# Kernel optimization log

Measured on AMD Instinct MI355X. Metric: run time of the kernel, lower is better.

## Reference

```python
import jax, jax.numpy as jnp
import numpy as np

H, DH, PE = 8, 64, 32
SCALE = DH ** -0.5


def setup_inputs() -> dict:
    key = jax.random.key(0)
    ks = jax.random.split(key, 12)
    B, L, D, K, G = 2, 4096, 256, 16, 4
    inner = H * DH
    kv_in = D + PE
    return {
        "spatial": jax.random.normal(ks[0], (B, L, D), jnp.float32),
        "topk_indices": jax.random.randint(ks[1], (B, L, K), 0, L, jnp.int32),
        "rpe": jax.random.normal(ks[2], (B, L, K, PE), jnp.float32),
        "self_rpe": jax.random.normal(ks[3], (B, L, 1, PE), jnp.float32),
        "distances": jax.random.uniform(ks[4], (B, L, K), jnp.float32) * 10.0,
        "global_latents": jax.random.normal(ks[5], (B, G, D), jnp.float32),
        "Wq": jax.random.normal(ks[6], (D, inner), jnp.float32) * (D ** -0.5),
        "Wk": jax.random.normal(ks[7], (kv_in, inner), jnp.float32) * (kv_in ** -0.5),
        "Wv": jax.random.normal(ks[8], (kv_in, inner), jnp.float32) * (kv_in ** -0.5),
        "Wo": jax.random.normal(ks[9], (inner, D), jnp.float32) * (inner ** -0.5),
        "bo": jnp.zeros((D,), jnp.float32),
        "log_sigma": jnp.full((H,), np.log(3.0), jnp.float32),
        "global_bias": jnp.zeros((), jnp.float32),
    }


def reference(spatial, topk_indices, rpe, self_rpe, distances, global_latents,
              Wq, Wk, Wv, Wo, bo, log_sigma, global_bias):
    B, L, D = spatial.shape
    k = topk_indices.shape[-1]
    G = global_latents.shape[1]
    dt = spatial.dtype

    # gather per-query neighbor features: [B, L, k, D]
    neighbors = jax.vmap(lambda s, idx: s[idx])(spatial, topk_indices)

    # context = [self, neighbors, globals] -> [B, L, c, D], c = 1 + k + G
    ctx = jnp.concatenate([
        spatial[:, :, None, :],
        neighbors,
        jnp.broadcast_to(global_latents[:, None, :, :], (B, L, G, D)),
    ], axis=2)

    # RPE concat on feature dim (self_rpe, rpe, zeros for globals)
    rpe_cat = jnp.concatenate([
        self_rpe, rpe, jnp.zeros((B, L, G, PE), dt)
    ], axis=2)
    ctx = jnp.concatenate([ctx, rpe_cat], axis=-1)  # [B, L, c, D+PE]

    Q = (spatial @ Wq).reshape(B, L, H, DH).transpose(0, 2, 1, 3)          # bhld
    Kt = (ctx @ Wk).reshape(B, L, 1 + k + G, H, DH).transpose(0, 3, 1, 2, 4)  # bhlcd
    Vt = (ctx @ Wv).reshape(B, L, 1 + k + G, H, DH).transpose(0, 3, 1, 2, 4)

    attn = jnp.einsum('bhld,bhlcd->bhlc', Q, Kt) * SCALE

    # gaussian distance bias on local (self + k neighbors) slots
    sigma_sq = jnp.exp(log_sigma) ** 2                     # [H]
    dist_local = jnp.concatenate([jnp.zeros((B, L, 1), dt), distances], axis=2)  # [B,L,1+k]
    gauss = -(dist_local ** 2)[:, None, :, :] / (2.0 * sigma_sq[None, :, None, None])
    bias = jnp.concatenate([
        gauss,
        jnp.broadcast_to(global_bias, (B, H, L, G)).astype(dt),
    ], axis=-1)
    attn = attn + bias

    w = jax.nn.softmax(attn, axis=-1)
    out = jnp.einsum('bhlc,bhlcd->bhld', w, Vt)
    out = out.transpose(0, 2, 1, 3).reshape(B, L, H * DH)
    return out @ Wo + bo
```

## Files before the change

### kernel.cpp

```cpp
#include <hip/hip_runtime.h>
#include <hip/hip_bf16.h>

#define BB 2
#define LL 4096
#define DD 256
#define KK 16
#define GG 4
#define HH 8
#define DH 64
#define PE 32
#define INNER 512
#define CC 21
#define MM (BB*LL)
#define SCALE 0.125f
#define NT1 1792
#define KT1 256
#define NT2 256
#define KT2 768

typedef unsigned short u16;
typedef __attribute__((ext_vector_type(8))) short bf16x8;
typedef __attribute__((ext_vector_type(4))) float f32x4;
typedef unsigned short ushort4_t __attribute__((ext_vector_type(4)));
typedef unsigned short ushort8_t __attribute__((ext_vector_type(8)));

static __device__ __forceinline__ float bf2f(unsigned short u) {
    return __uint_as_float(((unsigned)u) << 16);
}
static __device__ __forceinline__ unsigned short f2bf(float f) {
    unsigned u = __float_as_uint(f);
    unsigned r = u + 0x7fffu + ((u >> 16) & 1u);
    return (unsigned short)(r >> 16);
}
static __device__ __forceinline__ void gld_lds16(const void* g, void* l) {
    __builtin_amdgcn_global_load_lds(
        (const __attribute__((address_space(1))) unsigned int*)g,
        (__attribute__((address_space(3))) unsigned int*)l, 16, 0, 0);
}

static __device__ __forceinline__ float red8_dpp(float x) {
    int xi = __float_as_int(x);
    x += __int_as_float(__builtin_amdgcn_update_dpp(0, xi, 0xB1, 0xF, 0xF, true));
    xi = __float_as_int(x);
    x += __int_as_float(__builtin_amdgcn_update_dpp(0, xi, 0x4E, 0xF, 0xF, true));
    xi = __float_as_int(x);
    x += __int_as_float(__builtin_amdgcn_update_dpp(0, xi, 0x141, 0xF, 0xF, true));
    return x;
}

__global__ __launch_bounds__(256) void megaprep1(
    const float* __restrict__ Wq, const float* __restrict__ Wk,
    const float* __restrict__ Wv, const float* __restrict__ Wo,
    const float* __restrict__ spatial, const float* __restrict__ gl,
    float* __restrict__ A, float* __restrict__ M2, u16* __restrict__ Sb,
    u16* __restrict__ Kg, u16* __restrict__ Vg)
{
    const int bid = blockIdx.x;
    const int tid = threadIdx.x;
    __shared__ float smem[INNER];

    if (bid < 256) {
        const int e = bid;
        smem[tid]       = Wq[e * INNER + tid];
        smem[tid + 256] = Wq[e * INNER + 256 + tid];
        __syncthreads();
        const int h = tid >> 5, p = tid & 31;
        const float* __restrict__ wr = &Wk[(size_t)(DD + p) * INNER + h * DH];
        const float* __restrict__ qh = &smem[h * DH];
        float s = 0.f;
        #pragma unroll 8
        for (int d = 0; d < DH; ++d) s += wr[d] * qh[d];
        A[e * 256 + tid] = s;
    } else if (bid < 512) {
        const int hp = bid - 256;
        const int h = hp >> 5, p = hp & 31;
        if (tid < DH) smem[tid] = Wv[(size_t)(DD + p) * INNER + h * DH + tid];
        __syncthreads();
        float s = 0.f;
        #pragma unroll 8
        for (int d = 0; d < DH; ++d) s += smem[d] * Wo[(size_t)(h * DH + d) * DD + tid];
        M2[hp * 256 + tid] = s;
    } else if (bid < 1536) {
        const size_t i = ((size_t)(bid - 512) * 256 + tid) * 8;
        float4 a = *reinterpret_cast<const float4*>(&spatial[i]);
        float4 b = *reinterpret_cast<const float4*>(&spatial[i + 4]);
        ushort8_t v = { f2bf(a.x), f2bf(a.y), f2bf(a.z), f2bf(a.w),
                        f2bf(b.x), f2bf(b.y), f2bf(b.z), f2bf(b.w) };
        *reinterpret_cast<ushort8_t*>(&Sb[i]) = v;
    } else {
        const int local = bid - 1536;
        const int bg = local >> 2;
        const int col = (local & 3) * 128 + (tid & 127);
        const bool isv = tid >= 128;
        const float* __restrict__ W = isv ? Wv : Wk;
        const float* __restrict__ x = &gl[bg * DD];
        float s = 0.f;
        #pragma unroll 4
        for (int k = 0; k < DD; ++k) s += x[k] * W[(size_t)k * INNER + col];
        if (isv) Vg[bg * INNER + col] = f2bf(s);
        else     Kg[bg * INNER + col] = f2bf(s);
    }
}

__global__ __launch_bounds__(256) void megaprep2(
    const float* __restrict__ Wq, const float* __restrict__ Wk,
    const float* __restrict__ Wv, const float* __restrict__ A,
    const float* __restrict__ Wo, const float* __restrict__ M2,
    u16* __restrict__ Wt, u16* __restrict__ Wot)
{
    __shared__ float tile[64][65];
    const int bid = blockIdx.x;
    const int tid = threadIdx.x;

    const float* src; int ld, nloc, n0, k0, ldo; u16* dstbase; int kt;
    if (bid < 112) {
        n0 = (bid % 28) * 64; k0 = (bid / 28) * 64;
        if (n0 < 512)       { src = Wq; ld = INNER; nloc = n0; }
        else if (n0 < 1024) { src = Wk; ld = INNER; nloc = n0 - 512; }
        else if (n0 < 1536) { src = Wv; ld = INNER; nloc = n0 - 1024; }
        else                { src = A;  ld = 256;   nloc = n0 - 1536; }
        dstbase = Wt; ldo = KT1; kt = k0;
    } else {
        const int local = bid - 112;
        n0 = (local % 4) * 64; k0 = (local / 4) * 64;
        if (k0 < 512) { src = Wo; kt = k0; }
        else          { src = M2; kt = k0 - 512; }
        ld = DD; nloc = n0;
        dstbase = Wot; ldo = KT2;
    }

    const int tk = tid >> 4;
    const int tn = (tid & 15) * 4;
    #pragma unroll
    for (int rep = 0; rep < 4; ++rep) {
        const int k = kt + tk + rep * 16;
        float4 v = *reinterpret_cast<const float4*>(&src[(size_t)k * ld + nloc + tn]);
        tile[tk + rep * 16][tn + 0] = v.x; tile[tk + rep * 16][tn + 1] = v.y;
        tile[tk + rep * 16][tn + 2] = v.z; tile[tk + rep * 16][tn + 3] = v.w;
    }
    __syncthreads();
    const int wn = tid >> 2;
    const int wk = (tid & 3) * 16;
    ushort8_t o0, o1;
    #pragma unroll
    for (int i = 0; i < 8; ++i) o0[i] = f2bf(tile[wk + i][wn]);
    #pragma unroll
    for (int i = 0; i < 8; ++i) o1[i] = f2bf(tile[wk + 8 + i][wn]);
    u16* dst = &dstbase[(size_t)(n0 + wn) * ldo + k0 + wk];
    *reinterpret_cast<ushort8_t*>(dst)     = o0;
    *reinterpret_cast<ushort8_t*>(dst + 8) = o1;
}

template<int KT, int LDA, int NTOT, int BN, bool F32OUT>
__global__ __launch_bounds__(256) void mfma_gemm(
    const u16* __restrict__ A, const u16* __restrict__ Bt,
    u16* __restrict__ outB, float* __restrict__ outF,
    const float* __restrict__ bias)
{
    constexpr int WNT = BN / 2;
    constexpr int BJ  = WNT / 16;
    constexpr int BCH = BN / 8;

    __shared__ u16 As[128 * 64];
    __shared__ u16 Bs[BN * 64];

    const int tid  = threadIdx.x;
    const int lane = tid & 63;
    const int w    = tid >> 6;
    const int wr   = w >> 1, wc = w & 1;
    const int m0 = blockIdx.x * 128;
    const int n0 = blockIdx.y * BN;
    const int fr = lane & 15, fq = lane >> 4;

    f32x4 acc[4][BJ];
    #pragma unroll
    for (int i = 0; i < 4; ++i)
        #pragma unroll
        for (int j = 0; j < BJ; ++j)
            acc[i][j] = (f32x4){0.f, 0.f, 0.f, 0.f};

    for (int t = 0; t < KT / 64; ++t) {
        const int k0 = t * 64;
        #pragma unroll
        for (int cc = 0; cc < 4; ++cc) {
            const int chunk = w + cc * 4;
            gld_lds16(A + (size_t)(m0 + chunk * 8 + (lane >> 3)) * LDA + k0 + (lane & 7) * 8,
                      (char*)&As[0] + chunk * 1024);
        }
        #pragma unroll
        for (int cc = 0; cc < BCH / 4; ++cc) {
            const int chunk = w + cc * 4;
            gld_lds16(Bt + (size_t)(n0 + chunk * 8 + (lane >> 3)) * KT + k0 + (lane & 7) * 8,
                      (char*)&Bs[0] + chunk * 1024);
        }
        __syncthreads();
        #pragma unroll
        for (int ks = 0; ks < 2; ++ks) {
            bf16x8 av[4], bv[BJ];
            #pragma unroll
            for (int i = 0; i < 4; ++i)
                av[i] = *reinterpret_cast<const bf16x8*>(
                    &As[(wr * 64 + i * 16 + fr) * 64 + ks * 32 + fq * 8]);
            #pragma unroll
            for (int j = 0; j < BJ; ++j)
                bv[j] = *reinterpret_cast<const bf16x8*>(
                    &Bs[(wc * WNT + j * 16 + fr) * 64 + ks * 32 + fq * 8]);
            #pragma unroll
            for (int i = 0; i < 4; ++i)
                #pragma unroll
                for (int j = 0; j < BJ; ++j)
                    acc[i][j] = __builtin_amdgcn_mfma_f32_16x16x32_bf16(
                        av[i], bv[j], acc[i][j], 0, 0, 0);
        }
        __syncthreads();
    }

    #pragma unroll
    for (int i = 0; i < 4; ++i)
        #pragma unroll
        for (int j = 0; j < BJ; ++j)
            #pragma unroll
            for (int rgi = 0; rgi < 4; ++rgi) {
                const int row = m0 + wr * 64 + i * 16 + fq * 4 + rgi;
                const int col = n0 + wc * WNT + j * 16 + fr;
                if constexpr (F32OUT)
                    outF[(size_t)row * NTOT + col] = acc[i][j][rgi] + bias[col];
                else
                    outB[(size_t)row * NTOT + col] = f2bf(acc[i][j][rgi]);
            }
}

__global__ __launch_bounds__(256) void attn_kernel(
    const u16* __restrict__ X, const u16* __restrict__ Kg,
    const u16* __restrict__ Vg, const int* __restrict__ topk,
    const float* __restrict__ rpe, const float* __restrict__ self_rpe,
    const float* __restrict__ distances, const float* __restrict__ log_sigma,
    const float* __restrict__ global_bias, u16* __restrict__ ob2)
{
    const int lane = threadIdx.x & 63;
    const int bid  = blockIdx.x;
    const int xcd  = bid & 7;
    const int slot = bid >> 3;
    const int qblk = (xcd >> 2) * 1024 + slot * 4 + (xcd & 3);
    const int q = __builtin_amdgcn_readfirstlane(qblk * 4 + (threadIdx.x >> 6));
    const int b = q >> 12;
    const int h = lane >> 3;
    const int r = lane & 7;
    const int qk = q * KK;
    const size_t bL = (size_t)b * LL;
    const int bG = b * GG;

    float qf[8];
    {
        ushort8_t qv = *reinterpret_cast<const ushort8_t*>(&X[(size_t)q * NT1 + lane * 8]);
        #pragma unroll
        for (int j = 0; j < 8; ++j) qf[j] = bf2f(qv[j]);
    }
    float t4[4];
    {
        ushort4_t tu = *reinterpret_cast<const ushort4_t*>(
            &X[(size_t)q * NT1 + 1536 + h * 32 + r * 4]);
        t4[0] = bf2f(tu[0]); t4[1] = bf2f(tu[1]);
        t4[2] = bf2f(tu[2]); t4[3] = bf2f(tu[3]);
    }

    const float inv2sig = 0.5f * __expf(-2.f * log_sigma[h]);
    const float gbias   = global_bias[0];

    float denom = 0.f;
    float acc[8] = {0.f,0.f,0.f,0.f,0.f,0.f,0.f,0.f};
    float rb[4]  = {0.f,0.f,0.f,0.f};

    #pragma unroll
    for (int c = 0; c < CC; ++c) {
        const u16 *kb, *vb;
        const float* rp_ = nullptr;
        float biasc;
        if (c == 0) {
            kb = &X[(size_t)q * NT1 + 512];
            vb = &X[(size_t)q * NT1 + 1024];
            rp_ = &self_rpe[(size_t)q * PE];
            biasc = 0.f;
        } else if (c < 17) {
            const int idx = topk[qk + c - 1];
            kb = &X[(bL + idx) * NT1 + 512];
            vb = &X[(bL + idx) * NT1 + 1024];
            rp_ = &rpe[((size_t)qk + (c - 1)) * PE];
            const float d = distances[qk + c - 1];
            biasc = -(d * d) * inv2sig;
        } else {
            kb = &Kg[(size_t)(bG + c - 17) * INNER];
            vb = &Vg[(size_t)(bG + c - 17) * INNER];
            biasc = gbias;
        }
        ushort8_t kv = *reinterpret_cast<const ushort8_t*>(kb + lane * 8);
        ushort8_t vv = *reinterpret_cast<const ushort8_t*>(vb + lane * 8);
        float4 r4 = {0.f,0.f,0.f,0.f};
        if (c < 17) r4 = *reinterpret_cast<const float4*>(rp_ + r * 4);

        float part = bf2f(kv[0])*qf[0] + bf2f(kv[1])*qf[1]
                   + bf2f(kv[2])*qf[2] + bf2f(kv[3])*qf[3]
                   + bf2f(kv[4])*qf[4] + bf2f(kv[5])*qf[5]
                   + bf2f(kv[6])*qf[6] + bf2f(kv[7])*qf[7];
        if (c < 17)
            part += r4.x*t4[0] + r4.y*t4[1] + r4.z*t4[2] + r4.w*t4[3];
        part = red8_dpp(part);

        const float e = __expf(part * SCALE + biasc);
        denom += e;
        #pragma unroll
        for (int i = 0; i < 8; ++i) acc[i] += e * bf2f(vv[i]);
        if (c < 17) {
            rb[0] += e * r4.x; rb[1] += e * r4.y;
            rb[2] += e * r4.z; rb[3] += e * r4.w;
        }
    }

    const float inv = 1.f / denom;
    ushort4_t ru = { f2bf(rb[0]*inv), f2bf(rb[1]*inv), f2bf(rb[2]*inv), f2bf(rb[3]*inv) };
    *reinterpret_cast<ushort4_t*>(&ob2[(size_t)q * KT2 + 512 + h * 32 + r * 4]) = ru;
    ushort8_t ou = { f2bf(acc[0]*inv), f2bf(acc[1]*inv), f2bf(acc[2]*inv), f2bf(acc[3]*inv),
                     f2bf(acc[4]*inv), f2bf(acc[5]*inv), f2bf(acc[6]*inv), f2bf(acc[7]*inv) };
    *reinterpret_cast<ushort8_t*>(&ob2[(size_t)q * KT2 + lane * 8]) = ou;
}

extern "C" void kernel_launch(void* const* d_in, const int* in_sizes, int n_in,
                              void* d_out, int out_size, void* d_ws, size_t ws_size,
                              hipStream_t stream)
{
    const float* spatial     = (const float*)d_in[0];
    const int*   topk        = (const int*)  d_in[1];
    const float* rpe         = (const float*)d_in[2];
    const float* self_rpe    = (const float*)d_in[3];
    const float* distances   = (const float*)d_in[4];
    const float* gl          = (const float*)d_in[5];
    const float* Wq          = (const float*)d_in[6];
    const float* Wk          = (const float*)d_in[7];
    const float* Wv          = (const float*)d_in[8];
    const float* Wo          = (const float*)d_in[9];
    const float* bo          = (const float*)d_in[10];
    const float* log_sigma   = (const float*)d_in[11];
    const float* global_bias = (const float*)d_in[12];
    float* out = (float*)d_out;

    char* p = (char*)d_ws;
    float* A   = (float*)p;  p += (size_t)256 * 256 * 4;
    float* M2  = (float*)p;  p += (size_t)256 * 256 * 4;
    u16* Sb    = (u16*)p;    p += (size_t)MM * DD * 2;
    u16* Wt    = (u16*)p;    p += (size_t)NT1 * KT1 * 2;
    u16* Wot   = (u16*)p;    p += (size_t)NT2 * KT2 * 2;
    u16* X     = (u16*)p;    p += (size_t)MM * NT1 * 2;
    u16* ob2   = (u16*)p;    p += (size_t)MM * KT2 * 2;
    u16* Kg    = (u16*)p;    p += (size_t)BB * GG * INNER * 2;
    u16* Vg    = (u16*)p;    p += (size_t)BB * GG * INNER * 2;

    megaprep1<<<1568, 256, 0, stream>>>(Wq, Wk, Wv, Wo, spatial, gl,
                                        A, M2, Sb, Kg, Vg);
    megaprep2<<<160, 256, 0, stream>>>(Wq, Wk, Wv, A, Wo, M2, Wt, Wot);

    mfma_gemm<KT1, 256, NT1, 128, false><<<dim3(MM / 128, NT1 / 128), 256, 0, stream>>>(
        Sb, Wt, X, nullptr, nullptr);

    attn_kernel<<<MM / 4, 256, 0, stream>>>(
        X, Kg, Vg, topk, rpe, self_rpe, distances, log_sigma, global_bias, ob2);

    mfma_gemm<KT2, KT2, NT2, 32, true><<<dim3(MM / 128, NT2 / 32), 256, 0, stream>>>(
        ob2, Wot, nullptr, out, bo);
}
```

Baseline: 97.34 us.

## Merge weight-prep kernels and stage GEMM epilogue through swizzled LDS for vector stores

The two weight-preparation launches become one kernel. The A and M2 products are now written straight into the transposed bf16 weight buffers, which removes the intermediate fp32 arrays and one launch. The MFMA GEMM epilogue now writes accumulators into XOR-swizzled shared memory and reads them back as 16-byte vector stores, replacing scattered 2- or 4-byte global stores. This costs an extra LDS round trip and a barrier per block. The A-product writes are strided 2-byte stores into Wt.

```diff
diff --git a/kernel.cpp b/kernel.cpp
--- a/kernel.cpp
+++ b/kernel.cpp
@@ -48,38 +48,38 @@
     return x;
 }
 
-__global__ __launch_bounds__(256) void megaprep1(
+__global__ __launch_bounds__(256) void megaprep(
     const float* __restrict__ Wq, const float* __restrict__ Wk,
     const float* __restrict__ Wv, const float* __restrict__ Wo,
     const float* __restrict__ spatial, const float* __restrict__ gl,
-    float* __restrict__ A, float* __restrict__ M2, u16* __restrict__ Sb,
-    u16* __restrict__ Kg, u16* __restrict__ Vg)
+    u16* __restrict__ Sb, u16* __restrict__ Kg, u16* __restrict__ Vg,
+    u16* __restrict__ Wt, u16* __restrict__ Wot)
 {
+    __shared__ float shbuf[64 * 65];
     const int bid = blockIdx.x;
     const int tid = threadIdx.x;
-    __shared__ float smem[INNER];
 
     if (bid < 256) {
         const int e = bid;
-        smem[tid]       = Wq[e * INNER + tid];
-        smem[tid + 256] = Wq[e * INNER + 256 + tid];
+        shbuf[tid]       = Wq[e * INNER + tid];
+        shbuf[tid + 256] = Wq[e * INNER + 256 + tid];
         __syncthreads();
         const int h = tid >> 5, p = tid & 31;
         const float* __restrict__ wr = &Wk[(size_t)(DD + p) * INNER + h * DH];
-        const float* __restrict__ qh = &smem[h * DH];
+        const float* __restrict__ qh = &shbuf[h * DH];
         float s = 0.f;
         #pragma unroll 8
         for (int d = 0; d < DH; ++d) s += wr[d] * qh[d];
-        A[e * 256 + tid] = s;
+        Wt[(size_t)(1536 + tid) * KT1 + e] = f2bf(s);
     } else if (bid < 512) {
         const int hp = bid - 256;
         const int h = hp >> 5, p = hp & 31;
-        if (tid < DH) smem[tid] = Wv[(size_t)(DD + p) * INNER + h * DH + tid];
+        if (tid < DH) shbuf[tid] = Wv[(size_t)(DD + p) * INNER + h * DH + tid];
         __syncthreads();
         float s = 0.f;
         #pragma unroll 8
-        for (int d = 0; d < DH; ++d) s += smem[d] * Wo[(size_t)(h * DH + d) * DD + tid];
-        M2[hp * 256 + tid] = s;
+        for (int d = 0; d < DH; ++d) s += shbuf[d] * Wo[(size_t)(h * DH + d) * DD + tid];
+        Wot[(size_t)tid * KT2 + 512 + hp] = f2bf(s);
     } else if (bid < 1536) {
         const size_t i = ((size_t)(bid - 512) * 256 + tid) * 8;
         float4 a = *reinterpret_cast<const float4*>(&spatial[i]);
@@ -87,7 +87,7 @@
         ushort8_t v = { f2bf(a.x), f2bf(a.y), f2bf(a.z), f2bf(a.w),
                         f2bf(b.x), f2bf(b.y), f2bf(b.z), f2bf(b.w) };
         *reinterpret_cast<ushort8_t*>(&Sb[i]) = v;
-    } else {
+    } else if (bid < 1568) {
         const int local = bid - 1536;
         const int bg = local >> 2;
         const int col = (local & 3) * 128 + (tid & 127);
@@ -99,56 +99,43 @@
         for (int k = 0; k < DD; ++k) s += x[k] * W[(size_t)k * INNER + col];
         if (isv) Vg[bg * INNER + col] = f2bf(s);
         else     Kg[bg * INNER + col] = f2bf(s);
-    }
-}
-
-__global__ __launch_bounds__(256) void megaprep2(
-    const float* __restrict__ Wq, const float* __restrict__ Wk,
-    const float* __restrict__ Wv, const float* __restrict__ A,
-    const float* __restrict__ Wo, const float* __restrict__ M2,
-    u16* __restrict__ Wt, u16* __restrict__ Wot)
-{
-    __shared__ float tile[64][65];
-    const int bid = blockIdx.x;
-    const int tid = threadIdx.x;
-
-    const float* src; int ld, nloc, n0, k0, ldo; u16* dstbase; int kt;
-    if (bid < 112) {
-        n0 = (bid % 28) * 64; k0 = (bid / 28) * 64;
-        if (n0 < 512)       { src = Wq; ld = INNER; nloc = n0; }
-        else if (n0 < 1024) { src = Wk; ld = INNER; nloc = n0 - 512; }
-        else if (n0 < 1536) { src = Wv; ld = INNER; nloc = n0 - 1024; }
-        else                { src = A;  ld = 256;   nloc = n0 - 1536; }
-        dstbase = Wt; ldo = KT1; kt = k0;
     } else {
-        const int local = bid - 112;
-        n0 = (local % 4) * 64; k0 = (local / 4) * 64;
-        if (k0 < 512) { src = Wo; kt = k0; }
-        else          { src = M2; kt = k0 - 512; }
-        ld = DD; nloc = n0;
-        dstbase = Wot; ldo = KT2;
-    }
-
-    const int tk = tid >> 4;
-    const int tn = (tid & 15) * 4;
-    #pragma unroll
-    for (int rep = 0; rep < 4; ++rep) {
-        const int k = kt + tk + rep * 16;
-        float4 v = *reinterpret_cast<const float4*>(&src[(size_t)k * ld + nloc + tn]);
-        tile[tk + rep * 16][tn + 0] = v.x; tile[tk + rep * 16][tn + 1] = v.y;
-        tile[tk + rep * 16][tn + 2] = v.z; tile[tk + rep * 16][tn + 3] = v.w;
-    }
-    __syncthreads();
-    const int wn = tid >> 2;
-    const int wk = (tid & 3) * 16;
-    ushort8_t o0, o1;
-    #pragma unroll
-    for (int i = 0; i < 8; ++i) o0[i] = f2bf(tile[wk + i][wn]);
-    #pragma unroll
-    for (int i = 0; i < 8; ++i) o1[i] = f2bf(tile[wk + 8 + i][wn]);
-    u16* dst = &dstbase[(size_t)(n0 + wn) * ldo + k0 + wk];
-    *reinterpret_cast<ushort8_t*>(dst)     = o0;
-    *reinterpret_cast<ushort8_t*>(dst + 8) = o1;
+        float (*tile)[65] = reinterpret_cast<float (*)[65]>(shbuf);
+        const float* src; int ld, nloc, n0, k0, ldo; u16* dstbase; int kt;
+        if (bid < 1664) {
+            const int local = bid - 1568;
+            n0 = (local % 24) * 64; k0 = (local / 24) * 64;
+            if (n0 < 512)       { src = Wq; nloc = n0; }
+            else if (n0 < 1024) { src = Wk; nloc = n0 - 512; }
+            else                { src = Wv; nloc = n0 - 1024; }
+            ld = INNER; dstbase = Wt; ldo = KT1; kt = k0;
+        } else {
+            const int local = bid - 1664;
+            n0 = (local % 4) * 64; k0 = (local / 4) * 64;
+            src = Wo; ld = DD; nloc = n0; kt = k0;
+            dstbase = Wot; ldo = KT2;
+        }
+        const int tk = tid >> 4;
+        const int tn = (tid & 15) * 4;
+        #pragma unroll
+        for (int rep = 0; rep < 4; ++rep) {
+            const int k = kt + tk + rep * 16;
+            float4 v = *reinterpret_cast<const float4*>(&src[(size_t)k * ld + nloc + tn]);
+            tile[tk + rep * 16][tn + 0] = v.x; tile[tk + rep * 16][tn + 1] = v.y;
+            tile[tk + rep * 16][tn + 2] = v.z; tile[tk + rep * 16][tn + 3] = v.w;
+        }
+        __syncthreads();
+        const int wn = tid >> 2;
+        const int wk = (tid & 3) * 16;
+        ushort8_t o0, o1;
+        #pragma unroll
+        for (int i = 0; i < 8; ++i) o0[i] = f2bf(tile[wk + i][wn]);
+        #pragma unroll
+        for (int i = 0; i < 8; ++i) o1[i] = f2bf(tile[wk + 8 + i][wn]);
+        u16* dst = &dstbase[(size_t)(n0 + wn) * ldo + k0 + wk];
+        *reinterpret_cast<ushort8_t*>(dst)     = o0;
+        *reinterpret_cast<ushort8_t*>(dst + 8) = o1;
+    }
 }
 
 template<int KT, int LDA, int NTOT, int BN, bool F32OUT>
@@ -161,8 +148,9 @@
     constexpr int BJ  = WNT / 16;
     constexpr int BCH = BN / 8;
 
-    __shared__ u16 As[128 * 64];
-    __shared__ u16 Bs[BN * 64];
+    __shared__ uint32_t smem32[(128 * 64 + BN * 64) / 2];
+    u16* As = reinterpret_cast<u16*>(smem32);
+    u16* Bs = As + 128 * 64;
 
     const int tid  = threadIdx.x;
     const int lane = tid & 63;
@@ -185,13 +173,13 @@
         for (int cc = 0; cc < 4; ++cc) {
             const int chunk = w + cc * 4;
             gld_lds16(A + (size_t)(m0 + chunk * 8 + (lane >> 3)) * LDA + k0 + (lane & 7) * 8,
-                      (char*)&As[0] + chunk * 1024);
+                      (char*)As + chunk * 1024);
         }
         #pragma unroll
         for (int cc = 0; cc < BCH / 4; ++cc) {
             const int chunk = w + cc * 4;
             gld_lds16(Bt + (size_t)(n0 + chunk * 8 + (lane >> 3)) * KT + k0 + (lane & 7) * 8,
-                      (char*)&Bs[0] + chunk * 1024);
+                      (char*)Bs + chunk * 1024);
         }
         __syncthreads();
         #pragma unroll
@@ -215,19 +203,55 @@
         __syncthreads();
     }
 
-    #pragma unroll
-    for (int i = 0; i < 4; ++i)
-        #pragma unroll
-        for (int j = 0; j < BJ; ++j)
-            #pragma unroll
-            for (int rgi = 0; rgi < 4; ++rgi) {
-                const int row = m0 + wr * 64 + i * 16 + fq * 4 + rgi;
-                const int col = n0 + wc * WNT + j * 16 + fr;
-                if constexpr (F32OUT)
-                    outF[(size_t)row * NTOT + col] = acc[i][j][rgi] + bias[col];
-                else
-                    outB[(size_t)row * NTOT + col] = f2bf(acc[i][j][rgi]);
-            }
+    if constexpr (!F32OUT) {
+        u16* ep = As;
+        #pragma unroll
+        for (int i = 0; i < 4; ++i)
+            #pragma unroll
+            for (int j = 0; j < BJ; ++j)
+                #pragma unroll
+                for (int rgi = 0; rgi < 4; ++rgi) {
+                    const int rl = wr * 64 + i * 16 + fq * 4 + rgi;
+                    const int cl = wc * WNT + j * 16 + fr;
+                    const int cb = (cl >> 3) ^ ((rl >> 2) & (BN / 8 - 1));
+                    ep[rl * BN + (cb << 3) + (cl & 7)] = f2bf(acc[i][j][rgi]);
+                }
+        __syncthreads();
+        constexpr int PASS = (128 * BN) / (256 * 8);
+        #pragma unroll
+        for (int p = 0; p < PASS; ++p) {
+            const int flat = (p * 256 + tid) * 8;
+            const int rl = flat / BN, cl = flat % BN;
+            const int cb = (cl >> 3) ^ ((rl >> 2) & (BN / 8 - 1));
+            *reinterpret_cast<ushort8_t*>(&outB[(size_t)(m0 + rl) * NTOT + n0 + cl]) =
+                *reinterpret_cast<const ushort8_t*>(&ep[rl * BN + (cb << 3)]);
+        }
+    } else {
+        float* epf = reinterpret_cast<float*>(smem32);
+        #pragma unroll
+        for (int i = 0; i < 4; ++i)
+            #pragma unroll
+            for (int j = 0; j < BJ; ++j)
+                #pragma unroll
+                for (int rgi = 0; rgi < 4; ++rgi) {
+                    const int rl = wr * 64 + i * 16 + fq * 4 + rgi;
+                    const int cl = wc * WNT + j * 16 + fr;
+                    const int cb = (cl >> 2) ^ ((rl >> 2) & (BN / 4 - 1));
+                    epf[rl * BN + (cb << 2) + (cl & 3)] = acc[i][j][rgi];
+                }
+        __syncthreads();
+        constexpr int PASS = (128 * BN) / (256 * 4);
+        #pragma unroll
+        for (int p = 0; p < PASS; ++p) {
+            const int flat = (p * 256 + tid) * 4;
+            const int rl = flat / BN, cl = flat % BN;
+            const int cb = (cl >> 2) ^ ((rl >> 2) & (BN / 4 - 1));
+            float4 v = *reinterpret_cast<const float4*>(&epf[rl * BN + (cb << 2)]);
+            const float4 bb = *reinterpret_cast<const float4*>(&bias[n0 + cl]);
+            v.x += bb.x; v.y += bb.y; v.z += bb.z; v.w += bb.w;
+            *reinterpret_cast<float4*>(&outF[(size_t)(m0 + rl) * NTOT + n0 + cl]) = v;
+        }
+    }
 }
 
 __global__ __launch_bounds__(256) void attn_kernel(
@@ -344,8 +368,6 @@
     float* out = (float*)d_out;
 
     char* p = (char*)d_ws;
-    float* A   = (float*)p;  p += (size_t)256 * 256 * 4;
-    float* M2  = (float*)p;  p += (size_t)256 * 256 * 4;
     u16* Sb    = (u16*)p;    p += (size_t)MM * DD * 2;
     u16* Wt    = (u16*)p;    p += (size_t)NT1 * KT1 * 2;
     u16* Wot   = (u16*)p;    p += (size_t)NT2 * KT2 * 2;
@@ -354,9 +376,8 @@
     u16* Kg    = (u16*)p;    p += (size_t)BB * GG * INNER * 2;
     u16* Vg    = (u16*)p;    p += (size_t)BB * GG * INNER * 2;
 
-    megaprep1<<<1568, 256, 0, stream>>>(Wq, Wk, Wv, Wo, spatial, gl,
-                                        A, M2, Sb, Kg, Vg);
-    megaprep2<<<160, 256, 0, stream>>>(Wq, Wk, Wv, A, Wo, M2, Wt, Wot);
+    megaprep<<<1696, 256, 0, stream>>>(Wq, Wk, Wv, Wo, spatial, gl,
+                                       Sb, Kg, Vg, Wt, Wot);
 
     mfma_gemm<KT1, 256, NT1, 128, false><<<dim3(MM / 128, NT1 / 128), 256, 0, stream>>>(
         Sb, Wt, X, nullptr, nullptr);
```

Result: no change. 96.69 us (-0.7%).
